# Kernel optimization log

Hardware: AMD Instinct MI355X
Metric: run time of the kernel (lower is better)

## Reference

```python
import jax, jax.numpy as jnp
import numpy as np
from jax.scipy.linalg import expm

B, T, N_IN, N_HID, N_OUT = 8192, 2048, 2, 10, 10


def setup_inputs() -> dict:
    key = jax.random.key(0)
    k0, k1, k2, k3, k4 = jax.random.split(key, 5)
    inputs = jax.random.normal(k0, (B, T, N_IN), dtype=jnp.float32)
    # skew-symmetric seed for the orthogonal recurrent kernel (expm parametrization)
    A = jax.random.normal(k1, (N_HID, N_HID), dtype=jnp.float32) * 0.1
    # input_kernel: nn.Linear(n_inputs, n_hidden, bias=False) -> weight [H, D_in]
    W_in = jax.random.normal(k2, (N_HID, N_IN), dtype=jnp.float32) / np.sqrt(N_IN)
    # modrelu bias, initialized uniform(-0.01, 0.01) as in exprnn
    b_mod = jax.random.uniform(k3, (N_HID,), jnp.float32, -0.01, 0.01)
    # final nn.Linear(n_hidden, n_outputs)
    lin_W = jax.random.normal(k4, (N_OUT, N_HID), dtype=jnp.float32) / np.sqrt(N_HID)
    lin_b = jnp.zeros((N_OUT,), jnp.float32)
    return {"inputs": inputs, "A": A, "W_in": W_in, "b_mod": b_mod,
            "lin_W": lin_W, "lin_b": lin_b}


def _modrelu(z, b):
    # modrelu(z) = sign(z) * relu(|z| + b)
    return jnp.sign(z) * jax.nn.relu(jnp.abs(z) + b)


def reference(inputs, A, W_in, b_mod, lin_W, lin_b):
    # Orthogonal recurrent matrix: Bmat = expm(skew(A)), skew from strict upper triangle
    A_tri = jnp.triu(A, k=1)
    Bmat = expm(A_tri - A_tri.T)  # [H, H], orthogonal
    # Precompute input projections for all timesteps: [B, T, H]
    x_proj = jnp.einsum('btd,hd->bth', inputs, W_in)
    h0 = jnp.zeros((inputs.shape[0], W_in.shape[0]), dtype=inputs.dtype)

    def step(h, x_t):
        h_new = _modrelu(x_t + h @ Bmat, b_mod)
        return h_new, None

    hT, _ = jax.lax.scan(step, h0, jnp.swapaxes(x_proj, 0, 1))  # scan over time
    out = hT @ lin_W.T + lin_b  # [B, n_outputs]
    return out
```

## Files before the change

kernel.cpp:

```cpp
#include <hip/hip_runtime.h>

#define H 10
#define T_LEN 2048
#define BATCH 8192

#define MOVROR(x, K) __int_as_float(__builtin_amdgcn_mov_dpp(                    \
    __float_as_int(x), 0x120 + (K), 0xF, 0xF, true))

#define STR2(x) #x
#define VREG(n) "v" STR2(n)
#define DPP_(K) " row_ror:" STR2(K) " row_mask:0xf bank_mask:0xf\n\t"

#define STEP(X0, X1)                                                \
    "v_mul_f32 v54, " VREG(X0) ", %[w0]\n\t"                        \
    "v_fmac_f32 v54, " VREG(X1) ", %[w1]\n\t"                       \
    "v_fmac_f32 v54, %[h], %[b0]\n\t"                               \
    "v_mul_f32 v55, %[h], %[b4]" DPP_(4)                            \
    "v_mul_f32 v56, %[h], %[b8]" DPP_(8)                            \
    "v_mul_f32 v57, %[h], %[b12]" DPP_(12)                          \
    "v_fmac_f32 v54, %[h], %[b1]" DPP_(1)                           \
    "v_fmac_f32 v55, %[h], %[b5]" DPP_(5)                           \
    "v_fmac_f32 v56, %[h], %[b9]" DPP_(9)                           \
    "v_fmac_f32 v57, %[h], %[b13]" DPP_(13)                         \
    "v_fmac_f32 v54, %[h], %[b2]" DPP_(2)                           \
    "v_fmac_f32 v55, %[h], %[b6]" DPP_(6)                           \
    "v_fmac_f32 v56, %[h], %[b10]" DPP_(10)                         \
    "v_fmac_f32 v57, %[h], %[b14]" DPP_(14)                         \
    "v_fmac_f32 v54, %[h], %[b3]" DPP_(3)                           \
    "v_fmac_f32 v55, %[h], %[b7]" DPP_(7)                           \
    "v_fmac_f32 v56, %[h], %[b11]" DPP_(11)                         \
    "v_fmac_f32 v57, %[h], %[b15]" DPP_(15)                         \
    "v_add_f32 v54, v54, v55\n\t"                                   \
    "v_add_f32 v56, v56, v57\n\t"                                   \
    "v_add_f32 v54, v54, v56\n\t"                                   \
    "v_and_b32 v62, %[mk], v54\n\t"                                 \
    "v_add_f32 v62, v62, %[bm]\n\t"                                 \
    "v_max_f32 v62, 0, v62\n\t"                                     \
    "v_bfi_b32 %[h], %[mk], v62, v54\n\t"

#define SUBCTL(TAG, LD0, LD1, LD2, LD3)                             \
    "s_cmp_lt_u32 %[it], 253\n\t"                                   \
    "s_cbranch_scc0 Lsk" TAG "_%=\n\t"                              \
    "global_load_dwordx4 " LD0 ", v[60:61], off\n\t"                \
    "global_load_dwordx4 " LD1 ", v[60:61], off offset:16\n\t"      \
    "global_load_dwordx4 " LD2 ", v[60:61], off offset:32\n\t"      \
    "global_load_dwordx4 " LD3 ", v[60:61], off offset:48\n\t"      \
    "v_add_co_u32 v60, vcc, 64, v60\n\t"                            \
    "v_addc_co_u32 v61, vcc, 0, v61, vcc\n\t"                       \
    "s_waitcnt vmcnt(12)\n\t"                                       \
    "s_branch Ldn" TAG "_%=\n\t"                                    \
    "Lsk" TAG "_%=:\n\t"                                            \
    "s_waitcnt vmcnt(0)\n\t"                                        \
    "Ldn" TAG "_%=:\n\t"                                            \
    "s_add_i32 %[it], %[it], 1\n\t"

__global__ void expm_kernel(const float* __restrict__ A, float* __restrict__ Bout) {
    __shared__ double S[H][H];
    __shared__ double P[H][H];
    __shared__ double E[H][H];
    const int tid = threadIdx.x;
    const int i = tid / H, j = tid % H;
    if (tid < H * H) {
        double a = 0.0;
        if (i < j) a = (double)A[i * H + j];
        else if (i > j) a = -(double)A[j * H + i];
        a *= (1.0 / 256.0);
        S[i][j] = a;
        P[i][j] = a;
        E[i][j] = (i == j ? 1.0 : 0.0) + a;
    }
    __syncthreads();
    for (int k = 2; k <= 16; ++k) {
        double acc = 0.0;
        if (tid < H * H) {
            for (int m = 0; m < H; ++m) acc += P[i][m] * S[m][j];
            acc *= (1.0 / (double)k);
        }
        __syncthreads();
        if (tid < H * H) { P[i][j] = acc; E[i][j] += acc; }
        __syncthreads();
    }
    for (int rr = 0; rr < 8; ++rr) {
        double acc = 0.0;
        if (tid < H * H) {
            for (int m = 0; m < H; ++m) acc += E[i][m] * E[m][j];
        }
        __syncthreads();
        if (tid < H * H) E[i][j] = acc;
        __syncthreads();
    }
    if (tid < H * H) Bout[i * H + j] = (float)E[i][j];
}

__global__ __launch_bounds__(64, 2)
void rnn_kernel(const float* __restrict__ x,
                const float* __restrict__ Bm,
                const float* __restrict__ Win,
                const float* __restrict__ bmod,
                const float* __restrict__ lW,
                const float* __restrict__ lb,
                float* __restrict__ out) {
    const int lane = threadIdx.x;
    const int j    = lane & 15;
    const int row  = lane >> 4;
    const int bb   = blockIdx.x * 4 + row;

    float Bv[16];
#pragma unroll
    for (int k = 0; k < 16; ++k) {
        const int m = (j - k) & 15;
        Bv[k] = (j < H && m < H) ? Bm[m * H + j] : 0.f;
    }
    float w0j = 0.f, w1j = 0.f, bmj = 0.f;
    if (j < H) { w0j = Win[j * 2]; w1j = Win[j * 2 + 1]; bmj = bmod[j]; }

    float h = 0.f;
    int it = 0;
    const uint64_t addr = (uint64_t)(x + (size_t)bb * (T_LEN * 2));
    const unsigned alo = (unsigned)addr, ahi = (unsigned)(addr >> 32);

    asm volatile(
        "v_mov_b32 v60, %[alo]\n\t"
        "v_mov_b32 v61, %[ahi]\n\t"
        "global_load_dwordx4 v[64:67],   v[60:61], off\n\t"
        "global_load_dwordx4 v[68:71],   v[60:61], off offset:16\n\t"
        "global_load_dwordx4 v[72:75],   v[60:61], off offset:32\n\t"
        "global_load_dwordx4 v[76:79],   v[60:61], off offset:48\n\t"
        "global_load_dwordx4 v[80:83],   v[60:61], off offset:64\n\t"
        "global_load_dwordx4 v[84:87],   v[60:61], off offset:80\n\t"
        "global_load_dwordx4 v[88:91],   v[60:61], off offset:96\n\t"
        "global_load_dwordx4 v[92:95],   v[60:61], off offset:112\n\t"
        "global_load_dwordx4 v[96:99],   v[60:61], off offset:128\n\t"
        "global_load_dwordx4 v[100:103], v[60:61], off offset:144\n\t"
        "global_load_dwordx4 v[104:107], v[60:61], off offset:160\n\t"
        "global_load_dwordx4 v[108:111], v[60:61], off offset:176\n\t"
        "v_add_co_u32 v60, vcc, 0xc0, v60\n\t"
        "v_addc_co_u32 v61, vcc, 0, v61, vcc\n\t"
        "Lmain_%=:\n\t"
        SUBCTL("0", "v[112:115]", "v[116:119]", "v[120:123]", "v[124:127]")
        STEP(64, 65)  STEP(66, 67)  STEP(68, 69)  STEP(70, 71)
        STEP(72, 73)  STEP(74, 75)  STEP(76, 77)  STEP(78, 79)
        SUBCTL("1", "v[64:67]", "v[68:71]", "v[72:75]", "v[76:79]")
        STEP(80, 81)  STEP(82, 83)  STEP(84, 85)  STEP(86, 87)
        STEP(88, 89)  STEP(90, 91)  STEP(92, 93)  STEP(94, 95)
        SUBCTL("2", "v[80:83]", "v[84:87]", "v[88:91]", "v[92:95]")
        STEP(96, 97)  STEP(98, 99)  STEP(100, 101) STEP(102, 103)
        STEP(104, 105) STEP(106, 107) STEP(108, 109) STEP(110, 111)
        SUBCTL("3", "v[96:99]", "v[100:103]", "v[104:107]", "v[108:111]")
        STEP(112, 113) STEP(114, 115) STEP(116, 117) STEP(118, 119)
        STEP(120, 121) STEP(122, 123) STEP(124, 125) STEP(126, 127)
        "s_cmp_lg_u32 %[it], 256\n\t"
        "s_cbranch_scc1 Lmain_%=\n\t"
        : [h] "+v"(h), [it] "+s"(it)
        : [alo] "v"(alo), [ahi] "v"(ahi),
          [w0] "v"(w0j), [w1] "v"(w1j), [bm] "v"(bmj),
          [mk] "s"(0x7fffffffu),
          [b0] "v"(Bv[0]),  [b1] "v"(Bv[1]),  [b2] "v"(Bv[2]),  [b3] "v"(Bv[3]),
          [b4] "v"(Bv[4]),  [b5] "v"(Bv[5]),  [b6] "v"(Bv[6]),  [b7] "v"(Bv[7]),
          [b8] "v"(Bv[8]),  [b9] "v"(Bv[9]),  [b10] "v"(Bv[10]), [b11] "v"(Bv[11]),
          [b12] "v"(Bv[12]), [b13] "v"(Bv[13]), [b14] "v"(Bv[14]), [b15] "v"(Bv[15])
        : "memory", "vcc", "scc",
          "v54", "v55", "v56", "v57", "v60", "v61", "v62", "v63",
          "v64", "v65", "v66", "v67", "v68", "v69",
          "v70", "v71", "v72", "v73", "v74", "v75", "v76", "v77", "v78", "v79",
          "v80", "v81", "v82", "v83", "v84", "v85", "v86", "v87", "v88", "v89",
          "v90", "v91", "v92", "v93", "v94", "v95", "v96", "v97", "v98", "v99",
          "v100", "v101", "v102", "v103", "v104", "v105", "v106", "v107",
          "v108", "v109", "v110", "v111", "v112", "v113", "v114", "v115",
          "v116", "v117", "v118", "v119", "v120", "v121", "v122", "v123",
          "v124", "v125", "v126", "v127");

    float Lrot[16];
#pragma unroll
    for (int k = 0; k < 16; ++k) {
        const int m = (j - k) & 15;
        Lrot[k] = (j < H && m < H) ? lW[j * H + m] : 0.f;
    }
    float acc = (j < H) ? lb[j] : 0.f;
    acc = fmaf(h, Lrot[0], acc);
#define OUTK(K) { const float e_ = MOVROR(h, K); acc = fmaf(e_, Lrot[K], acc); }
    OUTK(1)  OUTK(2)  OUTK(3)  OUTK(4)  OUTK(5)
    OUTK(6)  OUTK(7)  OUTK(8)  OUTK(9)  OUTK(10)
    OUTK(11) OUTK(12) OUTK(13) OUTK(14) OUTK(15)
#undef OUTK
    if (j < H) out[(size_t)bb * H + j] = acc;
}

extern "C" void kernel_launch(void* const* d_in, const int* in_sizes, int n_in,
                              void* d_out, int out_size, void* d_ws, size_t ws_size,
                              hipStream_t stream) {
    const float* inputs = (const float*)d_in[0];
    const float* A      = (const float*)d_in[1];
    const float* W_in   = (const float*)d_in[2];
    const float* b_mod  = (const float*)d_in[3];
    const float* lin_W  = (const float*)d_in[4];
    const float* lin_b  = (const float*)d_in[5];
    float* out = (float*)d_out;
    float* Bmat = (float*)d_ws;

    expm_kernel<<<1, 128, 0, stream>>>(A, Bmat);
    rnn_kernel<<<BATCH / 4, 64, 0, stream>>>(inputs, Bmat, W_in, b_mod,
                                             lin_W, lin_b, out);
}
```

Baseline: 350.3 us.

## Fuse expm into RNN kernel and precompute DPP rotations with v_mov_dpp

Drops the separate single-block expm launch. Every RNN block now computes the matrix exponential redundantly in shared memory (double precision) before starting its recurrence, which removes a launch and a global round-trip but adds per-block prologue work. The per-step matvec is also restructured: fifteen DPP row-rotations of h are issued as v_mov_b32_dpp into registers, then plain FMAs run in two chains instead of four, and abs() is folded into the add. This trades DPP-modifier FMAs for separate moves plus FMAs, changing the latency profile of the serial recurrence.

```diff
diff --git a/kernel.cpp b/kernel.cpp
--- a/kernel.cpp
+++ b/kernel.cpp
@@ -12,31 +12,43 @@
 #define DPP_(K) " row_ror:" STR2(K) " row_mask:0xf bank_mask:0xf\n\t"
 
 #define STEP(X0, X1)                                                \
-    "v_mul_f32 v54, " VREG(X0) ", %[w0]\n\t"                        \
-    "v_fmac_f32 v54, " VREG(X1) ", %[w1]\n\t"                       \
-    "v_fmac_f32 v54, %[h], %[b0]\n\t"                               \
-    "v_mul_f32 v55, %[h], %[b4]" DPP_(4)                            \
-    "v_mul_f32 v56, %[h], %[b8]" DPP_(8)                            \
-    "v_mul_f32 v57, %[h], %[b12]" DPP_(12)                          \
-    "v_fmac_f32 v54, %[h], %[b1]" DPP_(1)                           \
-    "v_fmac_f32 v55, %[h], %[b5]" DPP_(5)                           \
-    "v_fmac_f32 v56, %[h], %[b9]" DPP_(9)                           \
-    "v_fmac_f32 v57, %[h], %[b13]" DPP_(13)                         \
-    "v_fmac_f32 v54, %[h], %[b2]" DPP_(2)                           \
-    "v_fmac_f32 v55, %[h], %[b6]" DPP_(6)                           \
-    "v_fmac_f32 v56, %[h], %[b10]" DPP_(10)                         \
-    "v_fmac_f32 v57, %[h], %[b14]" DPP_(14)                         \
-    "v_fmac_f32 v54, %[h], %[b3]" DPP_(3)                           \
-    "v_fmac_f32 v55, %[h], %[b7]" DPP_(7)                           \
-    "v_fmac_f32 v56, %[h], %[b11]" DPP_(11)                         \
-    "v_fmac_f32 v57, %[h], %[b15]" DPP_(15)                         \
-    "v_add_f32 v54, v54, v55\n\t"                                   \
+    "v_mul_f32 v56, " VREG(X0) ", %[w0]\n\t"                        \
+    "v_fmac_f32 v56, " VREG(X1) ", %[w1]\n\t"                       \
+    "v_fmac_f32 v56, %[h], %[b0]\n\t"                               \
+    "v_mov_b32_dpp v40, %[h]" DPP_(1)                               \
+    "v_mov_b32_dpp v41, %[h]" DPP_(2)                               \
+    "v_mov_b32_dpp v42, %[h]" DPP_(3)                               \
+    "v_mov_b32_dpp v43, %[h]" DPP_(4)                               \
+    "v_mov_b32_dpp v44, %[h]" DPP_(5)                               \
+    "v_mov_b32_dpp v45, %[h]" DPP_(6)                               \
+    "v_mov_b32_dpp v46, %[h]" DPP_(7)                               \
+    "v_mov_b32_dpp v47, %[h]" DPP_(8)                               \
+    "v_mov_b32_dpp v48, %[h]" DPP_(9)                               \
+    "v_mov_b32_dpp v49, %[h]" DPP_(10)                              \
+    "v_mov_b32_dpp v50, %[h]" DPP_(11)                              \
+    "v_mov_b32_dpp v51, %[h]" DPP_(12)                              \
+    "v_mov_b32_dpp v52, %[h]" DPP_(13)                              \
+    "v_mov_b32_dpp v53, %[h]" DPP_(14)                              \
+    "v_mov_b32_dpp v54, %[h]" DPP_(15)                              \
+    "v_mul_f32 v57, v47, %[b8]\n\t"                                 \
+    "v_fmac_f32 v56, v40, %[b1]\n\t"                                \
+    "v_fmac_f32 v57, v48, %[b9]\n\t"                                \
+    "v_fmac_f32 v56, v41, %[b2]\n\t"                                \
+    "v_fmac_f32 v57, v49, %[b10]\n\t"                               \
+    "v_fmac_f32 v56, v42, %[b3]\n\t"                                \
+    "v_fmac_f32 v57, v50, %[b11]\n\t"                               \
+    "v_fmac_f32 v56, v43, %[b4]\n\t"                                \
+    "v_fmac_f32 v57, v51, %[b12]\n\t"                               \
+    "v_fmac_f32 v56, v44, %[b5]\n\t"                                \
+    "v_fmac_f32 v57, v52, %[b13]\n\t"                               \
+    "v_fmac_f32 v56, v45, %[b6]\n\t"                                \
+    "v_fmac_f32 v57, v53, %[b14]\n\t"                               \
+    "v_fmac_f32 v56, v46, %[b7]\n\t"                                \
+    "v_fmac_f32 v57, v54, %[b15]\n\t"                               \
     "v_add_f32 v56, v56, v57\n\t"                                   \
-    "v_add_f32 v54, v54, v56\n\t"                                   \
-    "v_and_b32 v62, %[mk], v54\n\t"                                 \
-    "v_add_f32 v62, v62, %[bm]\n\t"                                 \
-    "v_max_f32 v62, 0, v62\n\t"                                     \
-    "v_bfi_b32 %[h], %[mk], v62, v54\n\t"
+    "v_add_f32 v57, abs(v56), %[bm]\n\t"                            \
+    "v_max_f32 v57, 0, v57\n\t"                                     \
+    "v_bfi_b32 %[h], %[mk], v57, v56\n\t"
 
 #define SUBCTL(TAG, LD0, LD1, LD2, LD3)                             \
     "s_cmp_lt_u32 %[it], 253\n\t"                                   \
@@ -54,62 +66,74 @@
     "Ldn" TAG "_%=:\n\t"                                            \
     "s_add_i32 %[it], %[it], 1\n\t"
 
-__global__ void expm_kernel(const float* __restrict__ A, float* __restrict__ Bout) {
-    __shared__ double S[H][H];
-    __shared__ double P[H][H];
-    __shared__ double E[H][H];
-    const int tid = threadIdx.x;
-    const int i = tid / H, j = tid % H;
-    if (tid < H * H) {
-        double a = 0.0;
-        if (i < j) a = (double)A[i * H + j];
-        else if (i > j) a = -(double)A[j * H + i];
-        a *= (1.0 / 256.0);
-        S[i][j] = a;
-        P[i][j] = a;
-        E[i][j] = (i == j ? 1.0 : 0.0) + a;
-    }
-    __syncthreads();
-    for (int k = 2; k <= 16; ++k) {
-        double acc = 0.0;
-        if (tid < H * H) {
-            for (int m = 0; m < H; ++m) acc += P[i][m] * S[m][j];
-            acc *= (1.0 / (double)k);
-        }
-        __syncthreads();
-        if (tid < H * H) { P[i][j] = acc; E[i][j] += acc; }
-        __syncthreads();
-    }
-    for (int rr = 0; rr < 8; ++rr) {
-        double acc = 0.0;
-        if (tid < H * H) {
-            for (int m = 0; m < H; ++m) acc += E[i][m] * E[m][j];
-        }
-        __syncthreads();
-        if (tid < H * H) E[i][j] = acc;
-        __syncthreads();
-    }
-    if (tid < H * H) Bout[i * H + j] = (float)E[i][j];
-}
-
 __global__ __launch_bounds__(64, 2)
 void rnn_kernel(const float* __restrict__ x,
-                const float* __restrict__ Bm,
+                const float* __restrict__ A,
                 const float* __restrict__ Win,
                 const float* __restrict__ bmod,
                 const float* __restrict__ lW,
                 const float* __restrict__ lb,
                 float* __restrict__ out) {
-    const int lane = threadIdx.x;
-    const int j    = lane & 15;
-    const int row  = lane >> 4;
+    __shared__ double S[H][H];
+    __shared__ double Pm[H][H];
+    __shared__ double E[H][H];
+    const int tid = threadIdx.x;
+
+    {
+        const int e0 = tid, e1 = tid + 64;
+        const int i0 = e0 / H, j0 = e0 % H;
+        const int i1 = e1 / H, j1 = e1 % H;
+        const bool v1 = (e1 < H * H);
+        double a0 = 0.0;
+        if (i0 < j0) a0 = (double)A[i0 * H + j0];
+        else if (i0 > j0) a0 = -(double)A[j0 * H + i0];
+        a0 *= (1.0 / 256.0);
+        S[i0][j0] = a0; Pm[i0][j0] = a0;
+        E[i0][j0] = (i0 == j0 ? 1.0 : 0.0) + a0;
+        if (v1) {
+            double a1 = 0.0;
+            if (i1 < j1) a1 = (double)A[i1 * H + j1];
+            else if (i1 > j1) a1 = -(double)A[j1 * H + i1];
+            a1 *= (1.0 / 256.0);
+            S[i1][j1] = a1; Pm[i1][j1] = a1;
+            E[i1][j1] = (i1 == j1 ? 1.0 : 0.0) + a1;
+        }
+        __syncthreads();
+        for (int k = 2; k <= 16; ++k) {
+            double t0 = 0.0, t1 = 0.0;
+            for (int m = 0; m < H; ++m) t0 += Pm[i0][m] * S[m][j0];
+            t0 *= (1.0 / (double)k);
+            if (v1) {
+                for (int m = 0; m < H; ++m) t1 += Pm[i1][m] * S[m][j1];
+                t1 *= (1.0 / (double)k);
+            }
+            __syncthreads();
+            Pm[i0][j0] = t0; E[i0][j0] += t0;
+            if (v1) { Pm[i1][j1] = t1; E[i1][j1] += t1; }
+            __syncthreads();
+        }
+        for (int rr = 0; rr < 8; ++rr) {
+            double t0 = 0.0, t1 = 0.0;
+            for (int m = 0; m < H; ++m) t0 += E[i0][m] * E[m][j0];
+            if (v1) {
+                for (int m = 0; m < H; ++m) t1 += E[i1][m] * E[m][j1];
+            }
+            __syncthreads();
+            E[i0][j0] = t0;
+            if (v1) E[i1][j1] = t1;
+            __syncthreads();
+        }
+    }
+
+    const int j    = tid & 15;
+    const int row  = tid >> 4;
     const int bb   = blockIdx.x * 4 + row;
 
     float Bv[16];
 #pragma unroll
     for (int k = 0; k < 16; ++k) {
         const int m = (j - k) & 15;
-        Bv[k] = (j < H && m < H) ? Bm[m * H + j] : 0.f;
+        Bv[k] = (j < H && m < H) ? (float)E[m][j] : 0.f;
     }
     float w0j = 0.f, w1j = 0.f, bmj = 0.f;
     if (j < H) { w0j = Win[j * 2]; w1j = Win[j * 2 + 1]; bmj = bmod[j]; }
@@ -160,7 +184,9 @@
           [b8] "v"(Bv[8]),  [b9] "v"(Bv[9]),  [b10] "v"(Bv[10]), [b11] "v"(Bv[11]),
           [b12] "v"(Bv[12]), [b13] "v"(Bv[13]), [b14] "v"(Bv[14]), [b15] "v"(Bv[15])
         : "memory", "vcc", "scc",
-          "v54", "v55", "v56", "v57", "v60", "v61", "v62", "v63",
+          "v40", "v41", "v42", "v43", "v44", "v45", "v46", "v47", "v48", "v49",
+          "v50", "v51", "v52", "v53", "v54", "v55", "v56", "v57",
+          "v60", "v61",
           "v64", "v65", "v66", "v67", "v68", "v69",
           "v70", "v71", "v72", "v73", "v74", "v75", "v76", "v77", "v78", "v79",
           "v80", "v81", "v82", "v83", "v84", "v85", "v86", "v87", "v88", "v89",
@@ -196,9 +222,8 @@
     const float* lin_W  = (const float*)d_in[4];
     const float* lin_b  = (const float*)d_in[5];
     float* out = (float*)d_out;
-    float* Bmat = (float*)d_ws;
-
-    expm_kernel<<<1, 128, 0, stream>>>(A, Bmat);
-    rnn_kernel<<<BATCH / 4, 64, 0, stream>>>(inputs, Bmat, W_in, b_mod,
+    (void)d_ws; (void)ws_size;
+
+    rnn_kernel<<<BATCH / 4, 64, 0, stream>>>(inputs, A, W_in, b_mod,
                                              lin_W, lin_b, out);
 }
```

After: 425.8 us. 1.22x slower.
